# Performance work log

Hardware: AMD Instinct MI355X
Metric: run time of the kernel (lower is better)

## Reference

```python
import jax, jax.numpy as jnp
import numpy as np


def setup_inputs() -> dict:
    key = jax.random.key(0)
    k1, k2 = jax.random.split(key)
    n_task, shot, feat, n_class = 32, 2048, 1024, 512
    inputs = jax.random.normal(k1, (n_task, shot, feat), dtype=jnp.float32)
    weights = jax.random.normal(k2, (n_task, n_class, feat), dtype=jnp.float32)
    return {"inputs": inputs, "weights": weights, "temp": 15}


def reference(inputs, weights, temp):
    # logits[t,s,c] = temp * (x.w - 0.5*||w||^2 - 0.5*||x||^2)
    dots = jnp.einsum('tsf,tcf->tsc', inputs, weights)        # [T,S,C]
    w_sq = 0.5 * jnp.sum(weights * weights, axis=2)           # [T,C]
    x_sq = 0.5 * jnp.sum(inputs * inputs, axis=2)             # [T,S]
    logits = temp * (dots - w_sq[:, None, :] - x_sq[:, :, None])
    return jnp.argmax(logits, axis=2)                         # [T,S] int
```

## Files before the change

### kernel.cpp

```cpp
#include <hip/hip_runtime.h>
#include <cstdint>
#include <cstddef>

#define T_TASKS 32
#define S_SHOT  2048
#define F_FEAT  1024
#define C_CLS   512
#define MARGIN  0.1f

typedef _Float16 f16;
typedef _Float16 f16x4 __attribute__((ext_vector_type(4)));
typedef _Float16 f16x8 __attribute__((ext_vector_type(8)));
typedef float    f32x4 __attribute__((ext_vector_type(4)));

__device__ __forceinline__ void gl_lds16(const void* g, void* l) {
  auto gp = (const __attribute__((address_space(1))) uint32_t*)(g);
  auto lp = (__attribute__((address_space(3))) uint32_t*)(l);
  __builtin_amdgcn_global_load_lds(gp, lp, 16, 0, 0);
}

__device__ __forceinline__ void upd3(float v, int i,
                                     float& v1, int& i1,
                                     float& v2, int& i2,
                                     float& v3, int& i3) {
  if (v > v1 || (v == v1 && i < i1)) { v3=v2; i3=i2; v2=v1; i2=i1; v1=v; i1=i; }
  else if (v > v2 || (v == v2 && i < i2)) { v3=v2; i3=i2; v2=v; i2=i; }
  else if (v > v3 || (v == v3 && i < i3)) { v3=v; i3=i; }
}

__global__ __launch_bounds__(256) void prep_w(const float* __restrict__ W,
                                              f16* __restrict__ Wh,
                                              float* __restrict__ wsq) {
  int rid = blockIdx.x * 4 + (threadIdx.x >> 6);
  int ln  = threadIdx.x & 63;
  int c   = rid & (C_CLS - 1);
  int t   = rid >> 9;
  const float* wr = W + (size_t)rid * F_FEAT;
  double s = 0.0;
#pragma unroll
  for (int j = 0; j < 4; ++j) {
    int f = (j * 64 + ln) * 4;
    float4 v = *(const float4*)(wr + f);
    s += (double)v.x * v.x + (double)v.y * v.y +
         (double)v.z * v.z + (double)v.w * v.w;
    f16x4 h;
    h.x = (f16)v.x; h.y = (f16)v.y; h.z = (f16)v.z; h.w = (f16)v.w;
    int kt = f >> 5;
    int q  = (f >> 3) & 3;
    int jj = f & 7;
    int u  = c * 4 + ((q + (c >> 1)) & 3);
    size_t off = ((size_t)(t * 32 + kt) << 14) + (size_t)u * 8 + jj;
    *(f16x4*)(Wh + off) = h;
  }
#pragma unroll
  for (int off = 32; off > 0; off >>= 1) s += __shfl_xor(s, off);
  if (ln == 0) wsq[rid] = (float)(0.5 * s);
}

__global__ __launch_bounds__(256, 2) void gemm_argmax(
    const float* __restrict__ X, const float* __restrict__ W,
    const f16* __restrict__ Wh, const float* __restrict__ wsq,
    int* __restrict__ out) {
  __shared__ __align__(16) f16 sWh[16384];
  __shared__ __align__(16) f16 sXh[64 * 40];
  __shared__ __align__(16) f16 sXl[64 * 40];
  __shared__ float swsq[C_CLS];
  __shared__ float cv[64][2][3];
  __shared__ int   ci[64][2][3];
  __shared__ int   amb_cnt;
  __shared__ int   amb_list[64];

  const int tid = threadIdx.x;
  const int wv  = tid >> 6, ln = tid & 63;
  const int rg  = wv >> 1, cg = wv & 1;
  const int m   = ln & 15, q = ln >> 4;
  const int bx  = blockIdx.x;
  const int t   = bx >> 5, rb = bx & 31;
  const int row0 = rb * 64;

  swsq[tid]       = wsq[t * C_CLS + tid];
  swsq[tid + 256] = wsq[t * C_CLS + tid + 256];
  if (tid == 0) amb_cnt = 0;

  const f32x4 zero4 = {0.f, 0.f, 0.f, 0.f};
  f32x4 acc[2][16];
#pragma unroll
  for (int a = 0; a < 2; ++a)
#pragma unroll
    for (int b = 0; b < 16; ++b) acc[a][b] = zero4;

  const float* Xblk = X + ((size_t)t * S_SHOT + row0) * F_FEAT;
  const f16*   Wht  = Wh + ((size_t)(t * 32) << 14);

  f16* aph = sXh + (rg * 32 + m) * 40 + q * 8;
  f16* apl = sXl + (rg * 32 + m) * 40 + q * 8;
  const int c0 = cg * 256 + m;
  const int u0 = c0 * 4 + ((q + (c0 >> 1)) & 3);
  const f16* bp = sWh + u0 * 8;

  for (int kt = 0; kt < 32; ++kt) {
    const f16* gW = Wht + (kt << 14) + wv * 4096 + ln * 8;
    f16* lW = sWh + wv * 4096;
#pragma unroll
    for (int i = 0; i < 8; ++i) gl_lds16(gW + i * 512, lW + i * 512);

#pragma unroll
    for (int j = 0; j < 2; ++j) {
      int idx = tid + j * 256;
      int r = idx >> 3, q4 = idx & 7;
      float4 v = *(const float4*)(Xblk + (size_t)r * F_FEAT + kt * 32 + q4 * 4);
      f16x4 h, l;
      h.x = (f16)v.x; l.x = (f16)(v.x - (float)h.x);
      h.y = (f16)v.y; l.y = (f16)(v.y - (float)h.y);
      h.z = (f16)v.z; l.z = (f16)(v.z - (float)h.z);
      h.w = (f16)v.w; l.w = (f16)(v.w - (float)h.w);
      *(f16x4*)(sXh + r * 40 + q4 * 4) = h;
      *(f16x4*)(sXl + r * 40 + q4 * 4) = l;
    }
    __syncthreads();

    f16x8 ah0 = *(const f16x8*)(aph);
    f16x8 ah1 = *(const f16x8*)(aph + 16 * 40);
    f16x8 al0 = *(const f16x8*)(apl);
    f16x8 al1 = *(const f16x8*)(apl + 16 * 40);
#pragma unroll
    for (int ct = 0; ct < 16; ++ct) {
      f16x8 bh = *(const f16x8*)(bp + ct * 512);
      acc[0][ct] = __builtin_amdgcn_mfma_f32_16x16x32_f16(ah0, bh, acc[0][ct], 0, 0, 0);
      acc[0][ct] = __builtin_amdgcn_mfma_f32_16x16x32_f16(al0, bh, acc[0][ct], 0, 0, 0);
      acc[1][ct] = __builtin_amdgcn_mfma_f32_16x16x32_f16(ah1, bh, acc[1][ct], 0, 0, 0);
      acc[1][ct] = __builtin_amdgcn_mfma_f32_16x16x32_f16(al1, bh, acc[1][ct], 0, 0, 0);
    }
    __syncthreads();
  }

#pragma unroll
  for (int rt = 0; rt < 2; ++rt) {
#pragma unroll
    for (int rr = 0; rr < 4; ++rr) {
      float v1 = -3.4e38f, v2 = -3.4e38f, v3 = -3.4e38f;
      int   i1 = 0x7fffffff, i2 = 0x7fffffff, i3 = 0x7fffffff;
#pragma unroll
      for (int ct = 0; ct < 16; ++ct) {
        int cidx = c0 + ct * 16;
        float sc = acc[rt][ct][rr] - swsq[cidx];
        upd3(sc, cidx, v1, i1, v2, i2, v3, i3);
      }
      for (int off = 1; off < 16; off <<= 1) {
        float w1 = __shfl_xor(v1, off); int j1 = __shfl_xor(i1, off);
        float w2 = __shfl_xor(v2, off); int j2 = __shfl_xor(i2, off);
        float w3 = __shfl_xor(v3, off); int j3 = __shfl_xor(i3, off);
        upd3(w1, j1, v1, i1, v2, i2, v3, i3);
        upd3(w2, j2, v1, i1, v2, i2, v3, i3);
        upd3(w3, j3, v1, i1, v2, i2, v3, i3);
      }
      if (m == 0) {
        int row = rg * 32 + rt * 16 + q * 4 + rr;
        cv[row][cg][0] = v1; ci[row][cg][0] = i1;
        cv[row][cg][1] = v2; ci[row][cg][1] = i2;
        cv[row][cg][2] = v3; ci[row][cg][2] = i3;
      }
    }
  }
  __syncthreads();

  if (tid < 64) {
    float a1 = cv[tid][0][0]; int aj = ci[tid][0][0];
    float b1 = cv[tid][1][0]; int bj = ci[tid][1][0];
    float win, runner; int widx;
    if (a1 > b1 || (a1 == b1 && aj < bj)) {
      win = a1; widx = aj; runner = fmaxf(b1, cv[tid][0][1]);
    } else {
      win = b1; widx = bj; runner = fmaxf(a1, cv[tid][1][1]);
    }
    if (win - runner >= MARGIN) {
      out[t * S_SHOT + row0 + tid] = widx;
    } else {
      int p = atomicAdd(&amb_cnt, 1);
      amb_list[p] = tid;
    }
  }
  __syncthreads();

  int nA = amb_cnt;
  for (int a = wv; a < nA; a += 4) {
    int rl = amb_list[a];
    const float* xr = X + ((size_t)t * S_SHOT + row0 + rl) * F_FEAT;
    double best = -1.0e300; int bidx = 0x7fffffff;
    for (int g = 0; g < 2; ++g) {
      for (int k = 0; k < 3; ++k) {
        int cidx = ci[rl][g][k];
        const float* wr = W + ((size_t)t * C_CLS + cidx) * F_FEAT;
        double sd = 0.0, sw = 0.0;
        for (int j = 0; j < 16; ++j) {
          float xv = xr[ln + 64 * j];
          float wv2 = wr[ln + 64 * j];
          sd += (double)xv * (double)wv2;
          sw += (double)wv2 * (double)wv2;
        }
#pragma unroll
        for (int off = 32; off > 0; off >>= 1) {
          sd += __shfl_xor(sd, off);
          sw += __shfl_xor(sw, off);
        }
        double sc = sd - 0.5 * sw;
        if (sc > best || (sc == best && cidx < bidx)) { best = sc; bidx = cidx; }
      }
    }
    if (ln == 0) out[t * S_SHOT + row0 + rl] = bidx;
  }
}

extern "C" void kernel_launch(void* const* d_in, const int* in_sizes, int n_in,
                              void* d_out, int out_size, void* d_ws, size_t ws_size,
                              hipStream_t stream) {
  (void)in_sizes; (void)n_in; (void)out_size;
  const float* X = (const float*)d_in[0];
  const float* W = (const float*)d_in[1];
  const size_t wh_bytes = (size_t)T_TASKS * C_CLS * F_FEAT * sizeof(f16);
  const size_t need = wh_bytes + (size_t)T_TASKS * C_CLS * sizeof(float);
  if (ws_size < need) return;
  f16*   Wh  = (f16*)d_ws;
  float* wsq = (float*)((char*)d_ws + wh_bytes);
  int*   out = (int*)d_out;
  prep_w<<<T_TASKS * C_CLS / 4, 256, 0, stream>>>(W, Wh, wsq);
  gemm_argmax<<<T_TASKS * (S_SHOT / 64), 256, 0, stream>>>(X, W, Wh, wsq, out);
}
```

Before: 811.6 us.

## Drop LDS staging in GEMM, load operands directly into registers with prefetch

The GEMM loop no longer stages W and X through shared memory with per-tile barriers. Each lane now loads its MFMA fragments straight from global memory, prefetching the next X tile into registers, and reads pre-laid-out fp16 W fragments directly. prep_w is restructured so each block handles one (task, k-tile) and accumulates the half-norm with float atomics into a zeroed buffer. Block order is swapped so consecutive blocks belong to different tasks. This removes barrier and LDS traffic but adds global/L2 load pressure and register use. The norm is now summed in float instead of double, which could shift near-tie results.

```diff
diff --git a/kernel.cpp b/kernel.cpp
--- a/kernel.cpp
+++ b/kernel.cpp
@@ -9,15 +9,9 @@
 #define MARGIN  0.1f
 
 typedef _Float16 f16;
-typedef _Float16 f16x4 __attribute__((ext_vector_type(4)));
 typedef _Float16 f16x8 __attribute__((ext_vector_type(8)));
 typedef float    f32x4 __attribute__((ext_vector_type(4)));
 
-__device__ __forceinline__ void gl_lds16(const void* g, void* l) {
-  auto gp = (const __attribute__((address_space(1))) uint32_t*)(g);
-  auto lp = (__attribute__((address_space(3))) uint32_t*)(l);
-  __builtin_amdgcn_global_load_lds(gp, lp, 16, 0, 0);
-}
 
 __device__ __forceinline__ void upd3(float v, int i,
                                      float& v1, int& i1,
@@ -28,42 +22,51 @@
   else if (v > v3 || (v == v3 && i < i3)) { v3=v; i3=i; }
 }
 
-__global__ __launch_bounds__(256) void prep_w(const float* __restrict__ W,
+__device__ __forceinline__ void cvt8(float4 a, float4 b, f16x8& h, f16x8& l) {
+  float f[8] = {a.x, a.y, a.z, a.w, b.x, b.y, b.z, b.w};
+#pragma unroll
+  for (int j = 0; j < 8; ++j) {
+    f16 hj = (f16)f[j];
+    h[j] = hj;
+    l[j] = (f16)(f[j] - (float)hj);
+  }
+}
+
+__global__ __launch_bounds__(256) void zero_wsq(float* wsq) {
+  wsq[blockIdx.x * 256 + threadIdx.x] = 0.f;
+}
+
+__global__ __launch_bounds__(512) void prep_w(const float* __restrict__ W,
                                               f16* __restrict__ Wh,
                                               float* __restrict__ wsq) {
-  int rid = blockIdx.x * 4 + (threadIdx.x >> 6);
-  int ln  = threadIdx.x & 63;
-  int c   = rid & (C_CLS - 1);
-  int t   = rid >> 9;
-  const float* wr = W + (size_t)rid * F_FEAT;
-  double s = 0.0;
-#pragma unroll
-  for (int j = 0; j < 4; ++j) {
-    int f = (j * 64 + ln) * 4;
-    float4 v = *(const float4*)(wr + f);
-    s += (double)v.x * v.x + (double)v.y * v.y +
-         (double)v.z * v.z + (double)v.w * v.w;
-    f16x4 h;
-    h.x = (f16)v.x; h.y = (f16)v.y; h.z = (f16)v.z; h.w = (f16)v.w;
-    int kt = f >> 5;
-    int q  = (f >> 3) & 3;
-    int jj = f & 7;
-    int u  = c * 4 + ((q + (c >> 1)) & 3);
-    size_t off = ((size_t)(t * 32 + kt) << 14) + (size_t)u * 8 + jj;
-    *(f16x4*)(Wh + off) = h;
-  }
-#pragma unroll
-  for (int off = 32; off > 0; off >>= 1) s += __shfl_xor(s, off);
-  if (ln == 0) wsq[rid] = (float)(0.5 * s);
+  const int bx = blockIdx.x;
+  const int t = bx >> 5, kt = bx & 31;
+  const int c = threadIdx.x;
+  const float* wr = W + ((size_t)(t * C_CLS + c)) * F_FEAT + kt * 32;
+  float v[32];
+  float s = 0.f;
+#pragma unroll
+  for (int i = 0; i < 8; ++i) {
+    float4 x = *(const float4*)(wr + i * 4);
+    v[i*4+0] = x.x; v[i*4+1] = x.y; v[i*4+2] = x.z; v[i*4+3] = x.w;
+    s += x.x*x.x + x.y*x.y + x.z*x.z + x.w*x.w;
+  }
+  const int ct = c >> 4, m = c & 15;
+  f16* base = Wh + ((size_t)((t * 32 + kt) * 32 + ct)) * 512 + m * 8;
+#pragma unroll
+  for (int q = 0; q < 4; ++q) {
+    f16x8 h;
+#pragma unroll
+    for (int j = 0; j < 8; ++j) h[j] = (f16)v[q * 8 + j];
+    *(f16x8*)(base + q * 128) = h;
+  }
+  atomicAdd(&wsq[t * C_CLS + c], 0.5f * s);
 }
 
 __global__ __launch_bounds__(256, 2) void gemm_argmax(
     const float* __restrict__ X, const float* __restrict__ W,
     const f16* __restrict__ Wh, const float* __restrict__ wsq,
     int* __restrict__ out) {
-  __shared__ __align__(16) f16 sWh[16384];
-  __shared__ __align__(16) f16 sXh[64 * 40];
-  __shared__ __align__(16) f16 sXl[64 * 40];
   __shared__ float swsq[C_CLS];
   __shared__ float cv[64][2][3];
   __shared__ int   ci[64][2][3];
@@ -75,12 +78,13 @@
   const int rg  = wv >> 1, cg = wv & 1;
   const int m   = ln & 15, q = ln >> 4;
   const int bx  = blockIdx.x;
-  const int t   = bx >> 5, rb = bx & 31;
+  const int t   = bx & 31, rb = bx >> 5;
   const int row0 = rb * 64;
 
   swsq[tid]       = wsq[t * C_CLS + tid];
   swsq[tid + 256] = wsq[t * C_CLS + tid + 256];
   if (tid == 0) amb_cnt = 0;
+  __syncthreads();
 
   const f32x4 zero4 = {0.f, 0.f, 0.f, 0.f};
   f32x4 acc[2][16];
@@ -89,51 +93,42 @@
 #pragma unroll
     for (int b = 0; b < 16; ++b) acc[a][b] = zero4;
 
-  const float* Xblk = X + ((size_t)t * S_SHOT + row0) * F_FEAT;
-  const f16*   Wht  = Wh + ((size_t)(t * 32) << 14);
-
-  f16* aph = sXh + (rg * 32 + m) * 40 + q * 8;
-  f16* apl = sXl + (rg * 32 + m) * 40 + q * 8;
+  const float* x0 = X + ((size_t)(t * S_SHOT + row0 + rg * 32 + m)) * F_FEAT + q * 8;
+  const float* x1 = x0 + (size_t)16 * F_FEAT;
+  const f16* wt = Wh + ((size_t)t * 32 * 32 * 512) + (size_t)(cg * 16) * 512 + ln * 8;
+
+  float4 p0a = *(const float4*)(x0);
+  float4 p0b = *(const float4*)(x0 + 4);
+  float4 p1a = *(const float4*)(x1);
+  float4 p1b = *(const float4*)(x1 + 4);
+
+#pragma unroll 2
+  for (int kt = 0; kt < 32; ++kt) {
+    const int kn = (kt < 31) ? (kt + 1) : 31;
+    float4 n0a = *(const float4*)(x0 + kn * 32);
+    float4 n0b = *(const float4*)(x0 + kn * 32 + 4);
+    float4 n1a = *(const float4*)(x1 + kn * 32);
+    float4 n1b = *(const float4*)(x1 + kn * 32 + 4);
+
+    f16x8 ah0, al0, ah1, al1;
+    cvt8(p0a, p0b, ah0, al0);
+    cvt8(p1a, p1b, ah1, al1);
+
+    const f16* bp = wt + (size_t)kt * 16384;
+    f16x8 b[16];
+#pragma unroll
+    for (int i = 0; i < 16; ++i) b[i] = *(const f16x8*)(bp + i * 512);
+#pragma unroll
+    for (int i = 0; i < 16; ++i) {
+      acc[0][i] = __builtin_amdgcn_mfma_f32_16x16x32_f16(ah0, b[i], acc[0][i], 0, 0, 0);
+      acc[0][i] = __builtin_amdgcn_mfma_f32_16x16x32_f16(al0, b[i], acc[0][i], 0, 0, 0);
+      acc[1][i] = __builtin_amdgcn_mfma_f32_16x16x32_f16(ah1, b[i], acc[1][i], 0, 0, 0);
+      acc[1][i] = __builtin_amdgcn_mfma_f32_16x16x32_f16(al1, b[i], acc[1][i], 0, 0, 0);
+    }
+    p0a = n0a; p0b = n0b; p1a = n1a; p1b = n1b;
+  }
+
   const int c0 = cg * 256 + m;
-  const int u0 = c0 * 4 + ((q + (c0 >> 1)) & 3);
-  const f16* bp = sWh + u0 * 8;
-
-  for (int kt = 0; kt < 32; ++kt) {
-    const f16* gW = Wht + (kt << 14) + wv * 4096 + ln * 8;
-    f16* lW = sWh + wv * 4096;
-#pragma unroll
-    for (int i = 0; i < 8; ++i) gl_lds16(gW + i * 512, lW + i * 512);
-
-#pragma unroll
-    for (int j = 0; j < 2; ++j) {
-      int idx = tid + j * 256;
-      int r = idx >> 3, q4 = idx & 7;
-      float4 v = *(const float4*)(Xblk + (size_t)r * F_FEAT + kt * 32 + q4 * 4);
-      f16x4 h, l;
-      h.x = (f16)v.x; l.x = (f16)(v.x - (float)h.x);
-      h.y = (f16)v.y; l.y = (f16)(v.y - (float)h.y);
-      h.z = (f16)v.z; l.z = (f16)(v.z - (float)h.z);
-      h.w = (f16)v.w; l.w = (f16)(v.w - (float)h.w);
-      *(f16x4*)(sXh + r * 40 + q4 * 4) = h;
-      *(f16x4*)(sXl + r * 40 + q4 * 4) = l;
-    }
-    __syncthreads();
-
-    f16x8 ah0 = *(const f16x8*)(aph);
-    f16x8 ah1 = *(const f16x8*)(aph + 16 * 40);
-    f16x8 al0 = *(const f16x8*)(apl);
-    f16x8 al1 = *(const f16x8*)(apl + 16 * 40);
-#pragma unroll
-    for (int ct = 0; ct < 16; ++ct) {
-      f16x8 bh = *(const f16x8*)(bp + ct * 512);
-      acc[0][ct] = __builtin_amdgcn_mfma_f32_16x16x32_f16(ah0, bh, acc[0][ct], 0, 0, 0);
-      acc[0][ct] = __builtin_amdgcn_mfma_f32_16x16x32_f16(al0, bh, acc[0][ct], 0, 0, 0);
-      acc[1][ct] = __builtin_amdgcn_mfma_f32_16x16x32_f16(ah1, bh, acc[1][ct], 0, 0, 0);
-      acc[1][ct] = __builtin_amdgcn_mfma_f32_16x16x32_f16(al1, bh, acc[1][ct], 0, 0, 0);
-    }
-    __syncthreads();
-  }
-
 #pragma unroll
   for (int rt = 0; rt < 2; ++rt) {
 #pragma unroll
@@ -193,7 +188,7 @@
         const float* wr = W + ((size_t)t * C_CLS + cidx) * F_FEAT;
         double sd = 0.0, sw = 0.0;
         for (int j = 0; j < 16; ++j) {
-          float xv = xr[ln + 64 * j];
+          float xv  = xr[ln + 64 * j];
           float wv2 = wr[ln + 64 * j];
           sd += (double)xv * (double)wv2;
           sw += (double)wv2 * (double)wv2;
@@ -223,6 +218,7 @@
   f16*   Wh  = (f16*)d_ws;
   float* wsq = (float*)((char*)d_ws + wh_bytes);
   int*   out = (int*)d_out;
-  prep_w<<<T_TASKS * C_CLS / 4, 256, 0, stream>>>(W, Wh, wsq);
+  zero_wsq<<<T_TASKS * C_CLS / 256, 256, 0, stream>>>(wsq);
+  prep_w<<<T_TASKS * 32, 512, 0, stream>>>(W, Wh, wsq);
   gemm_argmax<<<T_TASKS * (S_SHOT / 64), 256, 0, stream>>>(X, W, Wh, wsq, out);
 }
```

Measured after the change: 883.0 us. 1.09x slower.
